# Performance work log

Hardware: AMD Instinct MI355X
Metric: run time of the kernel (lower is better)

## Reference

```python
import jax, jax.numpy as jnp
import numpy as np

H, W = 96, 96
NUM_ITERS = 5          # num_iterations from __init__
SXY_G, COMPAT_G = 3.0, 3.0    # addPairwiseGaussian(sxy=(3,3), compat=3)
SXY_B, SRGB, COMPAT_B = 50.0, 20.0, 10.0  # addPairwiseBilateral(sxy=50, srgb=20, compat=10)
EPS = 1e-8


def _crf_marginals(img, m):
    """Exact dense mean-field CRF (the math pydensecrf approximates via
    permutohedral lattice). img: [H,W] float, m: [H,W] int in {0,1}.
    Returns Q: [2, N] marginals."""
    Hh, Ww = img.shape
    N = Hh * Ww
    # --- unary (replicates the source exactly, including the label swap) ---
    onehot0 = (m == 0).astype(jnp.float32)
    unary_p = jnp.stack([1.0 - onehot0, onehot0]).reshape(2, -1)   # [2, N]
    unary = -jnp.log(jnp.clip(unary_p, EPS, 1.0))
    # --- pairwise kernel: 3 * gaussian + 10 * bilateral, self-excluded ---
    ys, xs = jnp.meshgrid(jnp.arange(Hh, dtype=jnp.float32),
                          jnp.arange(Ww, dtype=jnp.float32), indexing='ij')
    pos = jnp.stack([xs.ravel(), ys.ravel()], axis=-1)             # [N, 2]
    f = img.reshape(-1)                                            # [N]
    d2 = jnp.sum((pos[:, None, :] - pos[None, :, :]) ** 2, axis=-1)  # [N, N] spatial sq dist
    # grayscale image duplicated into 2 feature channels -> 2 * (f_i - f_j)^2
    df2 = 2.0 * (f[:, None] - f[None, :]) ** 2                     # [N, N]
    K = (COMPAT_G * jnp.exp(-d2 / (2.0 * SXY_G ** 2))
         + COMPAT_B * jnp.exp(-d2 / (2.0 * SXY_B ** 2) - df2 / (2.0 * SRGB ** 2)))
    idx = jnp.arange(N)
    K = K.at[idx, idx].set(0.0)  # exclude self-interaction
    # --- mean-field iterations (Potts compatibility, 2 labels) ---
    Q = jax.nn.softmax(-unary, axis=0)  # [2, N]
    for _ in range(NUM_ITERS):
        msg = Q @ K                     # [2, N]; K is symmetric
        pairwise = msg[::-1]            # Potts: penalty from the OTHER label
        Q = jax.nn.softmax(-unary - pairwise, axis=0)
    return Q


def setup_inputs() -> dict:
    key = jax.random.key(0)
    k1, k2 = jax.random.split(key)
    image = jax.random.uniform(k1, (1, 1, H, W), dtype=jnp.float32) * 255.0
    mask = jax.random.randint(k2, (1, 1, H, W), 0, 2)
    return {"image": image, "mask": mask}


def reference(image, mask):
    img = image[0, 0]
    m = mask[0, 0]
    Q = _crf_marginals(img, m)
    pred = jnp.argmax(Q, axis=0).reshape(img.shape)
    return pred[None, None].astype(jnp.float32)   # [1,1,H,W]
```

## Files before the change

kernel.cpp:

```cpp
#include <hip/hip_runtime.h>

constexpr int W    = 96;
constexpr int NPIX = 9216;
constexpr int NM   = 35;
constexpr int NPKB = 18;
constexpr int NP   = 19;

constexpr float LCLIP = 18.420681f;

__global__ __launch_bounds__(256) void k_init(const float* __restrict__ img,
                                              float4* __restrict__ B4){
    int px = blockIdx.x*256 + threadIdx.x;
    float th = img[px] * 0.0122718463f;
    float c[72];
    c[0] = 1.f; c[71] = 0.f;
    #pragma unroll
    for (int m = 1; m <= NM; ++m){
        float s, co;
        sincosf((float)m*th, &s, &co);
        c[m]    = co;
        c[NM+m] = s;
    }
    #pragma unroll
    for (int p = 0; p < NPKB; ++p)
        B4[(size_t)p*NPIX + px] = make_float4(c[4*p], c[4*p+1], c[4*p+2], c[4*p+3]);
}

template<int MODE>
__global__ __launch_bounds__(384) void k_H(const int* __restrict__ mask,
        const float4* __restrict__ B4,
        const float* __restrict__ partV, const float* __restrict__ partVk,
        float* __restrict__ ksum, const float* __restrict__ qprev, float* __restrict__ qcur,
        float4* __restrict__ H4T, float* __restrict__ H3T,
        float4* __restrict__ H4Tk, float* __restrict__ H3Tk)
{
    __shared__ float4 P4[4][W];
    __shared__ float  qp[4][W];
    __shared__ float  tw50[193], tw3[193];
    const int  t    = threadIdx.x;
    const int  B    = blockIdx.x;
    const int  g0   = blockIdx.y;
    const bool ones = (MODE==0) && (g0 >= NP);
    const int  pack = ones ? g0 - NP : g0;
    const int  r    = t / W, xx = t - (t/W)*W;

    if (t < 193){
        float d = (float)(t - 96);
        tw50[t] = __expf(-d*d*(1.f/5000.f));
        tw3[t]  = __expf(-d*d*(1.f/18.f));
    }
    float A[4];
    if (pack < NPKB){
        #pragma unroll
        for (int j = 0; j < 4; ++j){
            int c = 4*pack + j;
            if (c == 0)       A[j] = 0.6923648f;
            else if (c <= 70){
                int m = (c <= NM) ? c : c - NM;
                A[j] = 1.3847296f * __expf(-0.0150598f*(float)(m*m));
            } else            A[j] = 0.f;
        }
    }

    {
        int px = B*384 + t;
        float q;
        if (ones){
            q = 1.f;
        } else if (MODE == 0){
            q = (mask[px]==0) ? 1.f/(1.f+__expf( LCLIP)) : 1.f/(1.f+__expf(-LCLIP));
        } else {
            float m = 0.f;
            #pragma unroll
            for (int p = 0; p < NP; ++p) m += partV[(size_t)p*NPIX + px];
            float kk;
            if (MODE == 1){
                kk = 0.f;
                #pragma unroll
                for (int p = 0; p < NP; ++p) kk += partVk[(size_t)p*NPIX + px];
                kk -= 13.f;
                if (g0 == 0) ksum[px] = kk;
            } else {
                kk = ksum[px];
            }
            float duv = (mask[px]==0) ? LCLIP : -LCLIP;
            float delta = duv + kk - 2.f*(m - 13.f*qprev[px]);
            q = 1.f/(1.f+__expf(delta));
        }
        if (!ones && g0 == 0) qcur[px] = q;
        if (pack < NPKB){
            float4 b = B4[(size_t)pack*NPIX + px];
            P4[r][xx] = make_float4(q*A[0]*b.x, q*A[1]*b.y, q*A[2]*b.z, q*A[3]*b.w);
        } else {
            qp[r][xx] = q;
        }
    }
    __syncthreads();

    const int x = xx, y = 4*B + r;
    if (pack < NPKB){
        float4 a = make_float4(0.f,0.f,0.f,0.f);
        #pragma unroll 4
        for (int xp = 0; xp < W; ++xp){
            float  w = tw50[x - xp + 96];
            float4 v = P4[r][xp];
            a.x = fmaf(w,v.x,a.x); a.y = fmaf(w,v.y,a.y);
            a.z = fmaf(w,v.z,a.z); a.w = fmaf(w,v.w,a.w);
        }
        (ones ? H4Tk : H4T)[(size_t)pack*NPIX + x*W + y] = a;
    } else {
        float h = 0.f;
        #pragma unroll 4
        for (int xp = 0; xp < W; ++xp)
            h = fmaf(tw3[x - xp + 96], qp[r][xp], h);
        (ones ? H3Tk : H3T)[x*W + y] = h;
    }
}

__global__ __launch_bounds__(384) void k_V(const float4* __restrict__ B4,
        const float4* __restrict__ H4T, const float4* __restrict__ H4Tk,
        const float* __restrict__ H3T, const float* __restrict__ H3Tk,
        float* __restrict__ partV, float* __restrict__ partVk)
{
    __shared__ float4 Hl[4][W];
    __shared__ float  Hl3[4][W];
    __shared__ float  tw50[193], tw3[193];
    const int  t    = threadIdx.x;
    const int  C    = blockIdx.x;
    const int  g0   = blockIdx.y;
    const bool ones = g0 >= NP;
    const int  pack = ones ? g0 - NP : g0;
    const int  r    = t / W, yy = t - (t/W)*W;

    if (t < 193){
        float d = (float)(t - 96);
        tw50[t] = __expf(-d*d*(1.f/5000.f));
        tw3[t]  = __expf(-d*d*(1.f/18.f));
    }
    if (pack < NPKB) Hl[r][yy]  = (ones ? H4Tk : H4T)[(size_t)pack*NPIX + (4*C+r)*W + yy];
    else             Hl3[r][yy] = (ones ? H3Tk : H3T)[(4*C+r)*W + yy];
    __syncthreads();

    const int yo = yy, x = 4*C + r, px = yo*W + x;
    float val;
    if (pack < NPKB){
        float4 a = make_float4(0.f,0.f,0.f,0.f);
        #pragma unroll 4
        for (int yp = 0; yp < W; ++yp){
            float  w = tw50[yo - yp + 96];
            float4 v = Hl[r][yp];
            a.x = fmaf(w,v.x,a.x); a.y = fmaf(w,v.y,a.y);
            a.z = fmaf(w,v.z,a.z); a.w = fmaf(w,v.w,a.w);
        }
        float4 b = B4[(size_t)pack*NPIX + px];
        val = a.x*b.x + a.y*b.y + a.z*b.z + a.w*b.w;
    } else {
        float ag = 0.f;
        #pragma unroll 4
        for (int yp = 0; yp < W; ++yp)
            ag = fmaf(tw3[yo - yp + 96], Hl3[r][yp], ag);
        val = 3.f * ag;
    }
    (ones ? partVk : partV)[(size_t)pack*NPIX + px] = val;
}

__global__ __launch_bounds__(256) void k_F(const int* __restrict__ mask,
        const float* __restrict__ partV, const float* __restrict__ ksum,
        const float* __restrict__ qprev, float* __restrict__ out){
    int px = blockIdx.x*256 + threadIdx.x;
    float m = 0.f;
    #pragma unroll
    for (int p = 0; p < NP; ++p) m += partV[(size_t)p*NPIX + px];
    float duv = (mask[px]==0) ? LCLIP : -LCLIP;
    float delta = duv + ksum[px] - 2.f*(m - 13.f*qprev[px]);
    out[px] = (delta > 0.f) ? 1.f : 0.f;
}

extern "C" void kernel_launch(void* const* d_in, const int* in_sizes, int n_in,
                              void* d_out, int out_size, void* d_ws, size_t ws_size,
                              hipStream_t stream){
    const float* img  = (const float*)d_in[0];
    const int*   mask = (const int*)d_in[1];
    float* out = (float*)d_out;
    float* ws  = (float*)d_ws;

    constexpr size_t TBL = (size_t)NPKB*NPIX*4;
    float4* B4    = (float4*)ws;
    float4* H4T   = (float4*)(ws + TBL);
    float4* H4Tk  = (float4*)(ws + 2*TBL);
    float*  base  = ws + 3*TBL;
    float* H3T   = base;
    float* H3Tk  = H3T  + NPIX;
    float* partV = H3Tk + NPIX;
    float* partVk= partV + (size_t)NP*NPIX;
    float* qA    = partVk + (size_t)NP*NPIX;
    float* qB    = qA + NPIX;
    float* ksum  = qB + NPIX;

    dim3 b(384);
    k_init<<<dim3(36), dim3(256), 0, stream>>>(img, B4);
    k_H<0><<<dim3(24,2*NP), b, 0, stream>>>(mask, B4, partV, partVk, ksum, qA, qA, H4T, H3T, H4Tk, H3Tk);
    k_V   <<<dim3(24,2*NP), b, 0, stream>>>(B4, H4T, H4Tk, H3T, H3Tk, partV, partVk);
    k_H<1><<<dim3(24,NP), b, 0, stream>>>(mask, B4, partV, partVk, ksum, qA, qB, H4T, H3T, H4Tk, H3Tk);
    k_V   <<<dim3(24,NP), b, 0, stream>>>(B4, H4T, H4Tk, H3T, H3Tk, partV, partVk);
    k_H<2><<<dim3(24,NP), b, 0, stream>>>(mask, B4, partV, partVk, ksum, qB, qA, H4T, H3T, H4Tk, H3Tk);
    k_V   <<<dim3(24,NP), b, 0, stream>>>(B4, H4T, H4Tk, H3T, H3Tk, partV, partVk);
    k_H<2><<<dim3(24,NP), b, 0, stream>>>(mask, B4, partV, partVk, ksum, qA, qB, H4T, H3T, H4Tk, H3Tk);
    k_V   <<<dim3(24,NP), b, 0, stream>>>(B4, H4T, H4Tk, H3T, H3Tk, partV, partVk);
    k_H<2><<<dim3(24,NP), b, 0, stream>>>(mask, B4, partV, partVk, ksum, qB, qA, H4T, H3T, H4Tk, H3Tk);
    k_V   <<<dim3(24,NP), b, 0, stream>>>(B4, H4T, H4Tk, H3T, H3Tk, partV, partVk);
    k_F<<<dim3(36), dim3(256), 0, stream>>>(mask, partV, ksum, qA, out);
}
```

Before: 88.92 us.

## Cut Fourier terms, tile 8 rows per block with dual outputs, recurrence sincos

Lowers the Fourier expansion of the bilateral range kernel from 35 to 31 harmonics, which cuts the pack count from 18 to 16 and the grid y size. Each H/V block now handles 8 rows or columns, and each thread computes two outputs that share one LDS value load, using padded shared memory. k_init builds the harmonics with an angle-addition recurrence instead of one sincos per harmonic. Fewer harmonics lowers approximation accuracy, and the recurrence can accumulate rounding error. The larger tiles also halve the number of blocks, which lowers parallelism.

```diff
diff --git a/kernel.cpp b/kernel.cpp
--- a/kernel.cpp
+++ b/kernel.cpp
@@ -2,9 +2,9 @@
 
 constexpr int W    = 96;
 constexpr int NPIX = 9216;
-constexpr int NM   = 35;
-constexpr int NPKB = 18;
-constexpr int NP   = 19;
+constexpr int NM   = 31;
+constexpr int NPKB = 16;
+constexpr int NP   = 17;
 
 constexpr float LCLIP = 18.420681f;
 
@@ -12,14 +12,18 @@
                                               float4* __restrict__ B4){
     int px = blockIdx.x*256 + threadIdx.x;
     float th = img[px] * 0.0122718463f;
-    float c[72];
-    c[0] = 1.f; c[71] = 0.f;
+    float c[64];
+    c[0] = 1.f; c[63] = 0.f;
+    float s1, c1;
+    sincosf(th, &s1, &c1);
+    float cm = 1.f, sm = 0.f;
     #pragma unroll
     for (int m = 1; m <= NM; ++m){
-        float s, co;
-        sincosf((float)m*th, &s, &co);
-        c[m]    = co;
-        c[NM+m] = s;
+        float cn = cm*c1 - sm*s1;
+        float sn = sm*c1 + cm*s1;
+        cm = cn; sm = sn;
+        c[m]    = cm;
+        c[NM+m] = sm;
     }
     #pragma unroll
     for (int p = 0; p < NPKB; ++p)
@@ -34,36 +38,37 @@
         float4* __restrict__ H4T, float* __restrict__ H3T,
         float4* __restrict__ H4Tk, float* __restrict__ H3Tk)
 {
-    __shared__ float4 P4[4][W];
-    __shared__ float  qp[4][W];
-    __shared__ float  tw50[193], tw3[193];
+    __shared__ float4 P4[8*97];
+    __shared__ float  qp[8*97];
+    __shared__ float  tw[193];
     const int  t    = threadIdx.x;
     const int  B    = blockIdx.x;
     const int  g0   = blockIdx.y;
     const bool ones = (MODE==0) && (g0 >= NP);
     const int  pack = ones ? g0 - NP : g0;
-    const int  r    = t / W, xx = t - (t/W)*W;
+    const bool G3   = (pack == NPKB);
 
     if (t < 193){
         float d = (float)(t - 96);
-        tw50[t] = __expf(-d*d*(1.f/5000.f));
-        tw3[t]  = __expf(-d*d*(1.f/18.f));
+        tw[t] = G3 ? __expf(-d*d*(1.f/18.f)) : __expf(-d*d*(1.f/5000.f));
     }
     float A[4];
-    if (pack < NPKB){
+    if (!G3){
         #pragma unroll
-        for (int j = 0; j < 4; ++j){
-            int c = 4*pack + j;
-            if (c == 0)       A[j] = 0.6923648f;
-            else if (c <= 70){
-                int m = (c <= NM) ? c : c - NM;
-                A[j] = 1.3847296f * __expf(-0.0150598f*(float)(m*m));
-            } else            A[j] = 0.f;
-        }
-    }
-
-    {
-        int px = B*384 + t;
+        for (int jj = 0; jj < 4; ++jj){
+            int cch = 4*pack + jj;
+            if (cch == 0)       A[jj] = 0.6923648f;
+            else if (cch <= 62){
+                int m = (cch <= NM) ? cch : cch - NM;
+                A[jj] = 1.3847296f * __expf(-0.0150598f*(float)(m*m));
+            } else              A[jj] = 0.f;
+        }
+    }
+
+    #pragma unroll
+    for (int k = 0; k < 2; ++k){
+        int l  = t + k*384;
+        int px = B*768 + l;
         float q;
         if (ones){
             q = 1.f;
@@ -88,32 +93,43 @@
             q = 1.f/(1.f+__expf(delta));
         }
         if (!ones && g0 == 0) qcur[px] = q;
-        if (pack < NPKB){
+        int ryl = l/96, xx = l - ryl*96;
+        if (!G3){
             float4 b = B4[(size_t)pack*NPIX + px];
-            P4[r][xx] = make_float4(q*A[0]*b.x, q*A[1]*b.y, q*A[2]*b.z, q*A[3]*b.w);
+            P4[ryl*97 + xx] = make_float4(q*A[0]*b.x, q*A[1]*b.y, q*A[2]*b.z, q*A[3]*b.w);
         } else {
-            qp[r][xx] = q;
+            qp[ryl*97 + xx] = q;
         }
     }
     __syncthreads();
 
-    const int x = xx, y = 4*B + r;
-    if (pack < NPKB){
-        float4 a = make_float4(0.f,0.f,0.f,0.f);
+    const int r = t & 7, xg = t >> 3;
+    const int y = 8*B + r;
+    if (!G3){
+        float4 a0 = make_float4(0.f,0.f,0.f,0.f), a1 = a0;
         #pragma unroll 4
         for (int xp = 0; xp < W; ++xp){
-            float  w = tw50[x - xp + 96];
-            float4 v = P4[r][xp];
-            a.x = fmaf(w,v.x,a.x); a.y = fmaf(w,v.y,a.y);
-            a.z = fmaf(w,v.z,a.z); a.w = fmaf(w,v.w,a.w);
-        }
-        (ones ? H4Tk : H4T)[(size_t)pack*NPIX + x*W + y] = a;
+            float4 v  = P4[r*97 + xp];
+            float  w0 = tw[xg - xp + 96];
+            float  w1 = tw[xg - xp + 96 + 48];
+            a0.x = fmaf(w0,v.x,a0.x); a0.y = fmaf(w0,v.y,a0.y);
+            a0.z = fmaf(w0,v.z,a0.z); a0.w = fmaf(w0,v.w,a0.w);
+            a1.x = fmaf(w1,v.x,a1.x); a1.y = fmaf(w1,v.y,a1.y);
+            a1.z = fmaf(w1,v.z,a1.z); a1.w = fmaf(w1,v.w,a1.w);
+        }
+        float4* dst = ones ? H4Tk : H4T;
+        dst[(size_t)pack*NPIX + xg*W      + y] = a0;
+        dst[(size_t)pack*NPIX + (xg+48)*W + y] = a1;
     } else {
-        float h = 0.f;
-        #pragma unroll 4
-        for (int xp = 0; xp < W; ++xp)
-            h = fmaf(tw3[x - xp + 96], qp[r][xp], h);
-        (ones ? H3Tk : H3T)[x*W + y] = h;
+        float h0 = 0.f, h1 = 0.f;
+        #pragma unroll 4
+        for (int xp = 0; xp < W; ++xp){
+            float qv = qp[r*97 + xp];
+            h0 = fmaf(tw[xg - xp + 96],      qv, h0);
+            h1 = fmaf(tw[xg - xp + 96 + 48], qv, h1);
+        }
+        float* dg = ones ? H3Tk : H3T;
+        dg[xg*W + y] = h0; dg[(xg+48)*W + y] = h1;
     }
 }
 
@@ -122,46 +138,61 @@
         const float* __restrict__ H3T, const float* __restrict__ H3Tk,
         float* __restrict__ partV, float* __restrict__ partVk)
 {
-    __shared__ float4 Hl[4][W];
-    __shared__ float  Hl3[4][W];
-    __shared__ float  tw50[193], tw3[193];
+    __shared__ float4 Hl[8*97];
+    __shared__ float  Hl3[8*97];
+    __shared__ float  tw[193];
     const int  t    = threadIdx.x;
     const int  C    = blockIdx.x;
     const int  g0   = blockIdx.y;
     const bool ones = g0 >= NP;
     const int  pack = ones ? g0 - NP : g0;
-    const int  r    = t / W, yy = t - (t/W)*W;
+    const bool G3   = (pack == NPKB);
 
     if (t < 193){
         float d = (float)(t - 96);
-        tw50[t] = __expf(-d*d*(1.f/5000.f));
-        tw3[t]  = __expf(-d*d*(1.f/18.f));
-    }
-    if (pack < NPKB) Hl[r][yy]  = (ones ? H4Tk : H4T)[(size_t)pack*NPIX + (4*C+r)*W + yy];
-    else             Hl3[r][yy] = (ones ? H3Tk : H3T)[(4*C+r)*W + yy];
+        tw[t] = G3 ? __expf(-d*d*(1.f/18.f)) : __expf(-d*d*(1.f/5000.f));
+    }
+    #pragma unroll
+    for (int k = 0; k < 2; ++k){
+        int l = t + k*384;
+        int col = l/96, yy = l - col*96;
+        if (!G3) Hl[col*97 + yy]  = (ones ? H4Tk : H4T)[(size_t)pack*NPIX + (8*C+col)*W + yy];
+        else     Hl3[col*97 + yy] = (ones ? H3Tk : H3T)[(8*C+col)*W + yy];
+    }
     __syncthreads();
 
-    const int yo = yy, x = 4*C + r, px = yo*W + x;
-    float val;
-    if (pack < NPKB){
-        float4 a = make_float4(0.f,0.f,0.f,0.f);
+    const int r = t & 7, yg = t >> 3;
+    const int x = 8*C + r;
+    if (!G3){
+        float4 a0 = make_float4(0.f,0.f,0.f,0.f), a1 = a0;
         #pragma unroll 4
         for (int yp = 0; yp < W; ++yp){
-            float  w = tw50[yo - yp + 96];
-            float4 v = Hl[r][yp];
-            a.x = fmaf(w,v.x,a.x); a.y = fmaf(w,v.y,a.y);
-            a.z = fmaf(w,v.z,a.z); a.w = fmaf(w,v.w,a.w);
-        }
-        float4 b = B4[(size_t)pack*NPIX + px];
-        val = a.x*b.x + a.y*b.y + a.z*b.z + a.w*b.w;
+            float4 v  = Hl[r*97 + yp];
+            float  w0 = tw[yg - yp + 96];
+            float  w1 = tw[yg - yp + 96 + 48];
+            a0.x = fmaf(w0,v.x,a0.x); a0.y = fmaf(w0,v.y,a0.y);
+            a0.z = fmaf(w0,v.z,a0.z); a0.w = fmaf(w0,v.w,a0.w);
+            a1.x = fmaf(w1,v.x,a1.x); a1.y = fmaf(w1,v.y,a1.y);
+            a1.z = fmaf(w1,v.z,a1.z); a1.w = fmaf(w1,v.w,a1.w);
+        }
+        int px0 = yg*W + x, px1 = (yg+48)*W + x;
+        float4 b0 = B4[(size_t)pack*NPIX + px0];
+        float4 b1 = B4[(size_t)pack*NPIX + px1];
+        float* dst = ones ? partVk : partV;
+        dst[(size_t)pack*NPIX + px0] = a0.x*b0.x + a0.y*b0.y + a0.z*b0.z + a0.w*b0.w;
+        dst[(size_t)pack*NPIX + px1] = a1.x*b1.x + a1.y*b1.y + a1.z*b1.z + a1.w*b1.w;
     } else {
-        float ag = 0.f;
-        #pragma unroll 4
-        for (int yp = 0; yp < W; ++yp)
-            ag = fmaf(tw3[yo - yp + 96], Hl3[r][yp], ag);
-        val = 3.f * ag;
-    }
-    (ones ? partVk : partV)[(size_t)pack*NPIX + px] = val;
+        float h0 = 0.f, h1 = 0.f;
+        #pragma unroll 4
+        for (int yp = 0; yp < W; ++yp){
+            float v = Hl3[r*97 + yp];
+            h0 = fmaf(tw[yg - yp + 96],      v, h0);
+            h1 = fmaf(tw[yg - yp + 96 + 48], v, h1);
+        }
+        float* dst = ones ? partVk : partV;
+        dst[(size_t)pack*NPIX + yg*W + x]      = 3.f*h0;
+        dst[(size_t)pack*NPIX + (yg+48)*W + x] = 3.f*h1;
+    }
 }
 
 __global__ __launch_bounds__(256) void k_F(const int* __restrict__ mask,
@@ -199,15 +230,15 @@
 
     dim3 b(384);
     k_init<<<dim3(36), dim3(256), 0, stream>>>(img, B4);
-    k_H<0><<<dim3(24,2*NP), b, 0, stream>>>(mask, B4, partV, partVk, ksum, qA, qA, H4T, H3T, H4Tk, H3Tk);
-    k_V   <<<dim3(24,2*NP), b, 0, stream>>>(B4, H4T, H4Tk, H3T, H3Tk, partV, partVk);
-    k_H<1><<<dim3(24,NP), b, 0, stream>>>(mask, B4, partV, partVk, ksum, qA, qB, H4T, H3T, H4Tk, H3Tk);
-    k_V   <<<dim3(24,NP), b, 0, stream>>>(B4, H4T, H4Tk, H3T, H3Tk, partV, partVk);
-    k_H<2><<<dim3(24,NP), b, 0, stream>>>(mask, B4, partV, partVk, ksum, qB, qA, H4T, H3T, H4Tk, H3Tk);
-    k_V   <<<dim3(24,NP), b, 0, stream>>>(B4, H4T, H4Tk, H3T, H3Tk, partV, partVk);
-    k_H<2><<<dim3(24,NP), b, 0, stream>>>(mask, B4, partV, partVk, ksum, qA, qB, H4T, H3T, H4Tk, H3Tk);
-    k_V   <<<dim3(24,NP), b, 0, stream>>>(B4, H4T, H4Tk, H3T, H3Tk, partV, partVk);
-    k_H<2><<<dim3(24,NP), b, 0, stream>>>(mask, B4, partV, partVk, ksum, qB, qA, H4T, H3T, H4Tk, H3Tk);
-    k_V   <<<dim3(24,NP), b, 0, stream>>>(B4, H4T, H4Tk, H3T, H3Tk, partV, partVk);
+    k_H<0><<<dim3(12,2*NP), b, 0, stream>>>(mask, B4, partV, partVk, ksum, qA, qA, H4T, H3T, H4Tk, H3Tk);
+    k_V   <<<dim3(12,2*NP), b, 0, stream>>>(B4, H4T, H4Tk, H3T, H3Tk, partV, partVk);
+    k_H<1><<<dim3(12,NP), b, 0, stream>>>(mask, B4, partV, partVk, ksum, qA, qB, H4T, H3T, H4Tk, H3Tk);
+    k_V   <<<dim3(12,NP), b, 0, stream>>>(B4, H4T, H4Tk, H3T, H3Tk, partV, partVk);
+    k_H<2><<<dim3(12,NP), b, 0, stream>>>(mask, B4, partV, partVk, ksum, qB, qA, H4T, H3T, H4Tk, H3Tk);
+    k_V   <<<dim3(12,NP), b, 0, stream>>>(B4, H4T, H4Tk, H3T, H3Tk, partV, partVk);
+    k_H<2><<<dim3(12,NP), b, 0, stream>>>(mask, B4, partV, partVk, ksum, qA, qB, H4T, H3T, H4Tk, H3Tk);
+    k_V   <<<dim3(12,NP), b, 0, stream>>>(B4, H4T, H4Tk, H3T, H3Tk, partV, partVk);
+    k_H<2><<<dim3(12,NP), b, 0, stream>>>(mask, B4, partV, partVk, ksum, qB, qA, H4T, H3T, H4Tk, H3Tk);
+    k_V   <<<dim3(12,NP), b, 0, stream>>>(B4, H4T, H4Tk, H3T, H3Tk, partV, partVk);
     k_F<<<dim3(36), dim3(256), 0, stream>>>(mask, partV, ksum, qA, out);
 }
```

Measured after the change: 80.67 us. 1.1x faster.
